# Performance work log

Hardware: AMD Instinct MI355X
Metric: run time of the kernel (lower is better)

The kernel has to match this reference:

```python
import jax, jax.numpy as jnp
import numpy as np

TEMPERATURE = 0.07
MASK_VAL = -9e15
EPS = 1e-8

def setup_inputs() -> dict:
    key = jax.random.key(0)
    features = jax.random.normal(key, (8192, 256), dtype=jnp.float32)
    return {"features": features}

def reference(features):
    # features: [N, D]
    N = features.shape[0]
    norm = jnp.linalg.norm(features, axis=-1, keepdims=True)
    f = features / jnp.maximum(norm, EPS)
    # cosine similarity via GEMM: [N, N]
    sim = f @ f.T
    idx = jnp.arange(N)
    # mask self-similarity BEFORE temperature scaling (as in the torch code)
    sim = jnp.where(idx[:, None] == idx[None, :], MASK_VAL, sim)
    sim = sim / TEMPERATURE
    # positive of row i is column (i - N//2) mod N (eye rolled by N//2 along dim 0)
    pos_col = (idx - N // 2) % N
    pos = sim[idx, pos_col]
    nll = -pos + jax.nn.logsumexp(sim, axis=-1)
    return nll.mean()
```

## Files before the change

### kernel.cpp

```cpp
#include <hip/hip_runtime.h>
#include <hip/hip_bf16.h>
#include <math.h>

#define N_ROWS 8192
#define D_DIM  256
#define HALF_N 4096
#define INV_T      14.285714285714286f
#define SCALE_LOG2 20.609929155556620f
#define NEG_SCALE  -20.609929155556620f
#define EPSV   1e-8f

typedef __attribute__((ext_vector_type(8))) short bf16x8;
typedef __attribute__((ext_vector_type(4))) float f32x4;

#define AS1 __attribute__((address_space(1)))
#define AS3 __attribute__((address_space(3)))

__device__ inline unsigned short f2bf(float x) {
    unsigned int u = __float_as_uint(x);
    unsigned int r = (u + 0x7fffu + ((u >> 16) & 1u)) >> 16;
    return (unsigned short)r;
}

__global__ __launch_bounds__(256) void k_norm(const float* __restrict__ feat,
                                              unsigned short* __restrict__ fbf,
                                              float* __restrict__ sumexp,
                                              float* __restrict__ out) {
    const int tid = threadIdx.x;
    const int gid = blockIdx.x * 256 + tid;
    if (gid < N_ROWS) sumexp[gid] = 0.f;
    if (gid == 0) out[0] = 0.f;

    const int w = tid >> 6, lane = tid & 63;
    const int row = blockIdx.x * 4 + w;
    const float4 v = ((const float4*)(feat + row * D_DIM))[lane];
    float ss = v.x*v.x + v.y*v.y + v.z*v.z + v.w*v.w;
    #pragma unroll
    for (int off = 32; off; off >>= 1) ss += __shfl_xor(ss, off);
    const float scale = 1.f / fmaxf(sqrtf(ss), EPSV);
    ushort4 o;
    o.x = f2bf(v.x * scale);
    o.y = f2bf(v.y * scale);
    o.z = f2bf(v.z * scale);
    o.w = f2bf(v.w * scale);
    ((ushort4*)(fbf + row * D_DIM))[lane] = o;
}

__global__ __launch_bounds__(256, 2) void k_sim(const unsigned short* __restrict__ fbf,
                                                float* __restrict__ sumexp) {
    __shared__ __align__(16) char Bs[16384];
    const int tid  = threadIdx.x;
    const int lane = tid & 63;
    const int w    = tid >> 6;
    const int q    = lane >> 4, l15 = lane & 15;

    int g          = (33 * blockIdx.x) >> 2;
    const int gEnd = (33 * (blockIdx.x + 1)) >> 2;

    const int tt0 = g >> 3;
    int rt = (int)((sqrtf(8.f * (float)tt0 + 1.f) - 1.f) * 0.5f);
    while ((rt + 1) * (rt + 2) / 2 <= tt0) ++rt;
    while (rt * (rt + 1) / 2 > tt0) --rt;
    int cs = tt0 - rt * (rt + 1) / 2;
    int jt = g & 7;

#define STAGE(colRow0) do {                                                   \
        const char* Bg_ = (const char*)fbf + (size_t)(colRow0) * 512;         \
        _Pragma("unroll")                                                     \
        for (int i_ = 0; i_ < 4; ++i_) {                                      \
            const int idx_ = i_ * 256 + tid;                                  \
            const int col_ = idx_ >> 5;                                       \
            const int cir_ = idx_ & 31;                                       \
            __builtin_amdgcn_global_load_lds(                                 \
                (const AS1 void*)(Bg_ + col_ * 512 + ((cir_ ^ (col_ & 7)) << 4)), \
                (AS3 void*)(Bs + idx_ * 16), 16, 0, 0);                       \
        }                                                                     \
    } while (0)

    bf16x8 afrag[8][4];
#define LOAD_A(rt_) do {                                                      \
        const int rowBase_ = (rt_) * 256 + w * 64;                            \
        _Pragma("unroll")                                                     \
        for (int t_ = 0; t_ < 8; ++t_)                                        \
            _Pragma("unroll")                                                 \
            for (int ri_ = 0; ri_ < 4; ++ri_)                                 \
                afrag[t_][ri_] = *(const bf16x8*)(fbf                         \
                    + (rowBase_ + ri_*16 + l15) * D_DIM + t_*32 + q*8);       \
    } while (0)

    float rsum[4][4];
#define ZERO_RSUM() do {                                                      \
        _Pragma("unroll")                                                     \
        for (int ri_ = 0; ri_ < 4; ++ri_)                                     \
            _Pragma("unroll")                                                 \
            for (int r_ = 0; r_ < 4; ++r_) rsum[ri_][r_] = 0.f;               \
    } while (0)

#define FLUSH_RSUM(rt_) do {                                                  \
        const int rowBase_ = (rt_) * 256 + w * 64;                            \
        _Pragma("unroll")                                                     \
        for (int ri_ = 0; ri_ < 4; ++ri_)                                     \
            _Pragma("unroll")                                                 \
            for (int r_ = 0; r_ < 4; ++r_) {                                  \
                float s_ = rsum[ri_][r_];                                     \
                s_ += __shfl_xor(s_, 1);                                      \
                s_ += __shfl_xor(s_, 2);                                      \
                s_ += __shfl_xor(s_, 4);                                      \
                s_ += __shfl_xor(s_, 8);                                      \
                if (l15 == 0)                                                 \
                    atomicAdd(&sumexp[rowBase_ + ri_ * 16 + q * 4 + r_], s_); \
            }                                                                 \
    } while (0)

    STAGE(cs * 256 + jt * 32);
    LOAD_A(rt);
    ZERO_RSUM();

    while (true) {
        const int colBase = cs * 256 + jt * 32;
        const bool isDiag = (rt == cs);
        const int rowBase = rt * 256 + w * 64;

        __syncthreads();

        f32x4 acc[4][2];
        #pragma unroll
        for (int ri = 0; ri < 4; ++ri)
            #pragma unroll
            for (int ci = 0; ci < 2; ++ci) acc[ri][ci] = (f32x4){0.f, 0.f, 0.f, 0.f};

        #pragma unroll
        for (int t = 0; t < 8; ++t) {
            bf16x8 bfrag[2];
            #pragma unroll
            for (int ci = 0; ci < 2; ++ci) {
                const int c   = ci * 16 + l15;
                const int cir = t * 4 + q;
                bfrag[ci] = *(const bf16x8*)(Bs + c * 512 + ((cir ^ (c & 7)) << 4));
            }
            #pragma unroll
            for (int ri = 0; ri < 4; ++ri)
                #pragma unroll
                for (int ci = 0; ci < 2; ++ci)
                    acc[ri][ci] = __builtin_amdgcn_mfma_f32_16x16x32_bf16(
                        afrag[t][ri], bfrag[ci], acc[ri][ci], 0, 0, 0);
        }

        const bool more = (g + 1 < gEnd);
        int nrt = rt, ncs = cs, njt = jt + 1;
        if (njt == 8) {
            njt = 0; ncs = cs + 1;
            if (ncs > rt) { nrt = rt + 1; ncs = 0; }
        }

        if (more) {
            __syncthreads();
            STAGE(ncs * 256 + njt * 32);
            if (njt == 0) LOAD_A(nrt);
        }

        if (isDiag) {
            #pragma unroll
            for (int ri = 0; ri < 4; ++ri) {
                const int trow = rowBase + ri * 16;
                #pragma unroll
                for (int ci = 0; ci < 2; ++ci) {
                    const int tcol = colBase + ci * 16;
                    if (trow == tcol) {
                        #pragma unroll
                        for (int r = 0; r < 4; ++r) {
                            const float e = __builtin_amdgcn_exp2f(
                                __builtin_fmaf(acc[ri][ci][r], SCALE_LOG2, NEG_SCALE));
                            rsum[ri][r] += (q * 4 + r == l15) ? 0.f : e;
                        }
                    } else {
                        #pragma unroll
                        for (int r = 0; r < 4; ++r)
                            rsum[ri][r] += __builtin_amdgcn_exp2f(
                                __builtin_fmaf(acc[ri][ci][r], SCALE_LOG2, NEG_SCALE));
                    }
                }
            }
        } else {
            float csum0 = 0.f, csum1 = 0.f;
            #pragma unroll
            for (int ri = 0; ri < 4; ++ri) {
                #pragma unroll
                for (int r = 0; r < 4; ++r) {
                    const float e0 = __builtin_amdgcn_exp2f(
                        __builtin_fmaf(acc[ri][0][r], SCALE_LOG2, NEG_SCALE));
                    const float e1 = __builtin_amdgcn_exp2f(
                        __builtin_fmaf(acc[ri][1][r], SCALE_LOG2, NEG_SCALE));
                    rsum[ri][r] += e0 + e1;
                    csum0 += e0;
                    csum1 += e1;
                }
            }
            csum0 += __shfl_xor(csum0, 16); csum0 += __shfl_xor(csum0, 32);
            csum1 += __shfl_xor(csum1, 16); csum1 += __shfl_xor(csum1, 32);
            if (q == 0)      atomicAdd(&sumexp[colBase      + l15], csum0);
            else if (q == 1) atomicAdd(&sumexp[colBase + 16 + l15], csum1);
        }

        if (!more) break;
        if (njt == 0) {
            FLUSH_RSUM(rt);
            ZERO_RSUM();
        }
        rt = nrt; cs = ncs; jt = njt; ++g;
    }

    FLUSH_RSUM(rt);
#undef STAGE
#undef LOAD_A
#undef ZERO_RSUM
#undef FLUSH_RSUM
}

__global__ __launch_bounds__(256) void k_nll(const float* __restrict__ feat,
                                             const float* __restrict__ sumexp,
                                             float* __restrict__ out) {
    __shared__ float red[4];
    const int tid = threadIdx.x, w = tid >> 6, lane = tid & 63;
    const int i  = blockIdx.x * 4 + w;
    const int pc = (i + HALF_N) & (N_ROWS - 1);
    const float4 a = ((const float4*)(feat + i  * D_DIM))[lane];
    const float4 b = ((const float4*)(feat + pc * D_DIM))[lane];
    float dab = a.x*b.x + a.y*b.y + a.z*b.z + a.w*b.w;
    float daa = a.x*a.x + a.y*a.y + a.z*a.z + a.w*a.w;
    float dbb = b.x*b.x + b.y*b.y + b.z*b.z + b.w*b.w;
    #pragma unroll
    for (int off = 32; off; off >>= 1) {
        dab += __shfl_xor(dab, off);
        daa += __shfl_xor(daa, off);
        dbb += __shfl_xor(dbb, off);
    }
    if (lane == 0) {
        const float pos = dab / (fmaxf(sqrtf(daa), EPSV) * fmaxf(sqrtf(dbb), EPSV));
        red[w] = INV_T + logf(sumexp[i]) - pos * INV_T;
    }
    __syncthreads();
    if (tid == 0)
        atomicAdd(out, (red[0] + red[1] + red[2] + red[3]) * (1.f / N_ROWS));
}

extern "C" void kernel_launch(void* const* d_in, const int* in_sizes, int n_in,
                              void* d_out, int out_size, void* d_ws, size_t ws_size,
                              hipStream_t stream) {
    const float* feat = (const float*)d_in[0];
    char* ws = (char*)d_ws;
    unsigned short* fbf = (unsigned short*)ws;
    float* sumexp = (float*)(ws + 4u * 1024u * 1024u);

    k_norm<<<N_ROWS / 4, 256, 0, stream>>>(feat, fbf, sumexp, (float*)d_out);
    k_sim <<<512,        256, 0, stream>>>(fbf, sumexp);
    k_nll <<<N_ROWS / 4, 256, 0, stream>>>(feat, sumexp, (float*)d_out);
}
```

Baseline: 124.2 us.

## Double-buffer B tiles in LDS and prefetch two tiles ahead with vmcnt waits

LDS for the B tile grows to two 16 KB buffers. Each iteration now computes from one buffer while the tile two steps ahead loads into the other. The per-iteration __syncthreads pair becomes a partial `s_waitcnt vmcnt(4)` plus raw barriers, so the in-flight global_load_lds for the next tile need not drain before the MFMA loop starts. The A-fragment reload for a new row tile now happens after the exp epilogue rather than overlapping it, and vmcnt also counts the atomics and A loads, so the partial wait may block more than intended.

```diff
diff --git a/kernel.cpp b/kernel.cpp
--- a/kernel.cpp
+++ b/kernel.cpp
@@ -48,7 +48,7 @@
 
 __global__ __launch_bounds__(256, 2) void k_sim(const unsigned short* __restrict__ fbf,
                                                 float* __restrict__ sumexp) {
-    __shared__ __align__(16) char Bs[16384];
+    __shared__ __align__(16) char Bs[32768];
     const int tid  = threadIdx.x;
     const int lane = tid & 63;
     const int w    = tid >> 6;
@@ -64,8 +64,16 @@
     int cs = tt0 - rt * (rt + 1) / 2;
     int jt = g & 7;
 
-#define STAGE(colRow0) do {                                                   \
+#define ADV(rt_, cs_, jt_) do {                                               \
+        if (++jt_ == 8) { jt_ = 0; if (++cs_ > rt_) { cs_ = 0; ++rt_; } }     \
+    } while (0)
+
+    int nrt = rt, ncs = cs, njt = jt;
+    ADV(nrt, ncs, njt);
+
+#define STAGE(colRow0, par) do {                                              \
         const char* Bg_ = (const char*)fbf + (size_t)(colRow0) * 512;         \
+        char* Bd_ = Bs + ((par) << 14);                                       \
         _Pragma("unroll")                                                     \
         for (int i_ = 0; i_ < 4; ++i_) {                                      \
             const int idx_ = i_ * 256 + tid;                                  \
@@ -73,7 +81,7 @@
             const int cir_ = idx_ & 31;                                       \
             __builtin_amdgcn_global_load_lds(                                 \
                 (const AS1 void*)(Bg_ + col_ * 512 + ((cir_ ^ (col_ & 7)) << 4)), \
-                (AS3 void*)(Bs + idx_ * 16), 16, 0, 0);                       \
+                (AS3 void*)(Bd_ + idx_ * 16), 16, 0, 0);                      \
         }                                                                     \
     } while (0)
 
@@ -112,16 +120,23 @@
             }                                                                 \
     } while (0)
 
-    STAGE(cs * 256 + jt * 32);
+    STAGE(cs * 256 + jt * 32, 0);
+    STAGE(ncs * 256 + njt * 32, 1);
     LOAD_A(rt);
     ZERO_RSUM();
 
+    int p = 0;
     while (true) {
         const int colBase = cs * 256 + jt * 32;
         const bool isDiag = (rt == cs);
         const int rowBase = rt * 256 + w * 64;
 
-        __syncthreads();
+        if (g + 1 < gEnd) asm volatile("s_waitcnt vmcnt(4)" ::: "memory");
+        else              asm volatile("s_waitcnt vmcnt(0)" ::: "memory");
+        __builtin_amdgcn_s_barrier();
+        __builtin_amdgcn_sched_barrier(0);
+
+        const char* Bp = Bs + (p << 14);
 
         f32x4 acc[4][2];
         #pragma unroll
@@ -136,7 +151,7 @@
             for (int ci = 0; ci < 2; ++ci) {
                 const int c   = ci * 16 + l15;
                 const int cir = t * 4 + q;
-                bfrag[ci] = *(const bf16x8*)(Bs + c * 512 + ((cir ^ (c & 7)) << 4));
+                bfrag[ci] = *(const bf16x8*)(Bp + c * 512 + ((cir ^ (c & 7)) << 4));
             }
             #pragma unroll
             for (int ri = 0; ri < 4; ++ri)
@@ -146,18 +161,13 @@
                         afrag[t][ri], bfrag[ci], acc[ri][ci], 0, 0, 0);
         }
 
+        __builtin_amdgcn_sched_barrier(0);
+        __builtin_amdgcn_s_barrier();
+
         const bool more = (g + 1 < gEnd);
-        int nrt = rt, ncs = cs, njt = jt + 1;
-        if (njt == 8) {
-            njt = 0; ncs = cs + 1;
-            if (ncs > rt) { nrt = rt + 1; ncs = 0; }
-        }
-
-        if (more) {
-            __syncthreads();
-            STAGE(ncs * 256 + njt * 32);
-            if (njt == 0) LOAD_A(nrt);
-        }
+        int rt2 = nrt, cs2 = ncs, jt2 = njt;
+        ADV(rt2, cs2, jt2);
+        if (g + 2 < gEnd) STAGE(cs2 * 256 + jt2 * 32, p);
 
         if (isDiag) {
             #pragma unroll
@@ -205,12 +215,16 @@
         if (!more) break;
         if (njt == 0) {
             FLUSH_RSUM(rt);
+            LOAD_A(nrt);
             ZERO_RSUM();
         }
-        rt = nrt; cs = ncs; jt = njt; ++g;
+        rt = nrt; cs = ncs; jt = njt;
+        nrt = rt2; ncs = cs2; njt = jt2;
+        p ^= 1; ++g;
     }
 
     FLUSH_RSUM(rt);
+#undef ADV
 #undef STAGE
 #undef LOAD_A
 #undef ZERO_RSUM
```

New measurement: 123.8 us. Within noise of the previous version (-0.3%).

## Fuse norm, similarity and NLL kernels into one persistent kernel with grid barriers

Applied to the files above, without the earlier changes.

Merges the three kernels into a single 512-block launch. Flag-based grid-wide barriers sit between the normalization, similarity/logsumexp and final NLL phases. This removes two kernel launches and their inter-kernel gaps. The cost is two spin-wait barriers, which rely on all 512 blocks being co-resident (2 per CU) and could deadlock otherwise. Flag reset relies on a sentinel and on cross-launch state in the workspace.

```diff
diff --git a/kernel.cpp b/kernel.cpp
--- a/kernel.cpp
+++ b/kernel.cpp
@@ -5,10 +5,12 @@
 #define N_ROWS 8192
 #define D_DIM  256
 #define HALF_N 4096
+#define NBLK   512
 #define INV_T      14.285714285714286f
 #define SCALE_LOG2 20.609929155556620f
 #define NEG_SCALE  -20.609929155556620f
 #define EPSV   1e-8f
+#define SENT   0x5AFEC0DEu
 
 typedef __attribute__((ext_vector_type(8))) short bf16x8;
 typedef __attribute__((ext_vector_type(4))) float f32x4;
@@ -22,40 +24,51 @@
     return (unsigned short)r;
 }
 
-__global__ __launch_bounds__(256) void k_norm(const float* __restrict__ feat,
-                                              unsigned short* __restrict__ fbf,
-                                              float* __restrict__ sumexp,
-                                              float* __restrict__ out) {
-    const int tid = threadIdx.x;
-    const int gid = blockIdx.x * 256 + tid;
-    if (gid < N_ROWS) sumexp[gid] = 0.f;
-    if (gid == 0) out[0] = 0.f;
-
-    const int w = tid >> 6, lane = tid & 63;
-    const int row = blockIdx.x * 4 + w;
-    const float4 v = ((const float4*)(feat + row * D_DIM))[lane];
-    float ss = v.x*v.x + v.y*v.y + v.z*v.z + v.w*v.w;
-    #pragma unroll
-    for (int off = 32; off; off >>= 1) ss += __shfl_xor(ss, off);
-    const float scale = 1.f / fmaxf(sqrtf(ss), EPSV);
-    ushort4 o;
-    o.x = f2bf(v.x * scale);
-    o.y = f2bf(v.y * scale);
-    o.z = f2bf(v.z * scale);
-    o.w = f2bf(v.w * scale);
-    ((ushort4*)(fbf + row * D_DIM))[lane] = o;
-}
-
-__global__ __launch_bounds__(256, 2) void k_sim(const unsigned short* __restrict__ fbf,
-                                                float* __restrict__ sumexp) {
+__global__ __launch_bounds__(256, 2) void k_all(const float* __restrict__ feat,
+                                                unsigned short* __restrict__ fbf,
+                                                float* __restrict__ sumexp,
+                                                unsigned int* __restrict__ flg1,
+                                                unsigned int* __restrict__ flg2,
+                                                float* __restrict__ out) {
     __shared__ __align__(16) char Bs[16384];
+    __shared__ float red[4];
     const int tid  = threadIdx.x;
+    const int b    = blockIdx.x;
     const int lane = tid & 63;
     const int w    = tid >> 6;
     const int q    = lane >> 4, l15 = lane & 15;
 
-    int g          = (33 * blockIdx.x) >> 2;
-    const int gEnd = (33 * (blockIdx.x + 1)) >> 2;
+    if (tid == 0)
+        __hip_atomic_store(&flg2[b], 0u, __ATOMIC_RELAXED, __HIP_MEMORY_SCOPE_AGENT);
+    #pragma unroll
+    for (int r = 0; r < 4; ++r) {
+        const int row = b * 16 + w * 4 + r;
+        const float4 v = ((const float4*)(feat + row * D_DIM))[lane];
+        float ss = v.x*v.x + v.y*v.y + v.z*v.z + v.w*v.w;
+        #pragma unroll
+        for (int off = 32; off; off >>= 1) ss += __shfl_xor(ss, off);
+        const float sc = 1.f / fmaxf(sqrtf(ss), EPSV);
+        ushort4 o;
+        o.x = f2bf(v.x * sc); o.y = f2bf(v.y * sc);
+        o.z = f2bf(v.z * sc); o.w = f2bf(v.w * sc);
+        ((ushort4*)(fbf + row * D_DIM))[lane] = o;
+    }
+    if (tid < 16) sumexp[b * 16 + tid] = 0.f;
+    if (b == 0 && tid == 0) out[0] = 0.f;
+
+    __syncthreads();
+    __threadfence();
+    if (tid == 0)
+        __hip_atomic_store(&flg1[b], SENT, __ATOMIC_RELEASE, __HIP_MEMORY_SCOPE_AGENT);
+    for (int j = tid; j < NBLK; j += 256)
+        while (__hip_atomic_load(&flg1[j], __ATOMIC_RELAXED, __HIP_MEMORY_SCOPE_AGENT) != SENT)
+            __builtin_amdgcn_s_sleep(2);
+    __syncthreads();
+    __threadfence();
+
+    {
+    int g          = (33 * b) >> 2;
+    const int gEnd = (33 * (b + 1)) >> 2;
 
     const int tt0 = g >> 3;
     int rt = (int)((sqrtf(8.f * (float)tt0 + 1.f) - 1.f) * 0.5f);
@@ -215,33 +228,46 @@
 #undef LOAD_A
 #undef ZERO_RSUM
 #undef FLUSH_RSUM
-}
-
-__global__ __launch_bounds__(256) void k_nll(const float* __restrict__ feat,
-                                             const float* __restrict__ sumexp,
-                                             float* __restrict__ out) {
-    __shared__ float red[4];
-    const int tid = threadIdx.x, w = tid >> 6, lane = tid & 63;
-    const int i  = blockIdx.x * 4 + w;
-    const int pc = (i + HALF_N) & (N_ROWS - 1);
-    const float4 a = ((const float4*)(feat + i  * D_DIM))[lane];
-    const float4 b = ((const float4*)(feat + pc * D_DIM))[lane];
-    float dab = a.x*b.x + a.y*b.y + a.z*b.z + a.w*b.w;
-    float daa = a.x*a.x + a.y*a.y + a.z*a.z + a.w*a.w;
-    float dbb = b.x*b.x + b.y*b.y + b.z*b.z + b.w*b.w;
+    }
+
+    __threadfence();
+    if (tid == 0)
+        __hip_atomic_store(&flg2[b], SENT, __ATOMIC_RELEASE, __HIP_MEMORY_SCOPE_AGENT);
+    for (int j = tid; j < NBLK; j += 256)
+        while (__hip_atomic_load(&flg2[j], __ATOMIC_RELAXED, __HIP_MEMORY_SCOPE_AGENT) != SENT)
+            __builtin_amdgcn_s_sleep(2);
+    __syncthreads();
+    __threadfence();
+
+    float wsum = 0.f;
     #pragma unroll
-    for (int off = 32; off; off >>= 1) {
-        dab += __shfl_xor(dab, off);
-        daa += __shfl_xor(daa, off);
-        dbb += __shfl_xor(dbb, off);
-    }
-    if (lane == 0) {
-        const float pos = dab / (fmaxf(sqrtf(daa), EPSV) * fmaxf(sqrtf(dbb), EPSV));
-        red[w] = INV_T + logf(sumexp[i]) - pos * INV_T;
-    }
-    __syncthreads();
-    if (tid == 0)
+    for (int r = 0; r < 4; ++r) {
+        const int i  = b * 16 + w * 4 + r;
+        const int pc = (i + HALF_N) & (N_ROWS - 1);
+        const float4 a = ((const float4*)(feat + i  * D_DIM))[lane];
+        const float4 c = ((const float4*)(feat + pc * D_DIM))[lane];
+        float dab = a.x*c.x + a.y*c.y + a.z*c.z + a.w*c.w;
+        float daa = a.x*a.x + a.y*a.y + a.z*a.z + a.w*a.w;
+        float dbb = c.x*c.x + c.y*c.y + c.z*c.z + c.w*c.w;
+        #pragma unroll
+        for (int off = 32; off; off >>= 1) {
+            dab += __shfl_xor(dab, off);
+            daa += __shfl_xor(daa, off);
+            dbb += __shfl_xor(dbb, off);
+        }
+        if (lane == 0) {
+            const float se = __hip_atomic_load(&sumexp[i], __ATOMIC_RELAXED,
+                                               __HIP_MEMORY_SCOPE_AGENT);
+            const float pos = dab / (fmaxf(sqrtf(daa), EPSV) * fmaxf(sqrtf(dbb), EPSV));
+            wsum += INV_T + logf(se) - pos * INV_T;
+        }
+    }
+    if (lane == 0) red[w] = wsum;
+    __syncthreads();
+    if (tid == 0) {
         atomicAdd(out, (red[0] + red[1] + red[2] + red[3]) * (1.f / N_ROWS));
+        __hip_atomic_store(&flg1[b], 0u, __ATOMIC_RELAXED, __HIP_MEMORY_SCOPE_AGENT);
+    }
 }
 
 extern "C" void kernel_launch(void* const* d_in, const int* in_sizes, int n_in,
@@ -250,9 +276,9 @@
     const float* feat = (const float*)d_in[0];
     char* ws = (char*)d_ws;
     unsigned short* fbf = (unsigned short*)ws;
-    float* sumexp = (float*)(ws + 4u * 1024u * 1024u);
-
-    k_norm<<<N_ROWS / 4, 256, 0, stream>>>(feat, fbf, sumexp, (float*)d_out);
-    k_sim <<<512,        256, 0, stream>>>(fbf, sumexp);
-    k_nll <<<N_ROWS / 4, 256, 0, stream>>>(feat, sumexp, (float*)d_out);
+    float* sumexp  = (float*)(ws + 4u * 1024u * 1024u);
+    unsigned int* flg1 = (unsigned int*)(ws + 4u * 1024u * 1024u + 32768u);
+    unsigned int* flg2 = flg1 + NBLK;
+
+    k_all<<<NBLK, 256, 0, stream>>>(feat, fbf, sumexp, flg1, flg2, (float*)d_out);
 }
```

After: 250.6 us. 2.02x slower.
